# Kernel tuning notes

Hardware: AMD Instinct MI355X
Metric: run time of the kernel (lower is better)

## Reference

```python
import jax, jax.numpy as jnp
import numpy as np

N = 8192
F_IN = 128
F_OUT = 128


def setup_inputs() -> dict:
    key = jax.random.key(0)
    k1, k2, k3, k4, k5 = jax.random.split(key, 5)
    x = jax.random.normal(k1, (N, F_IN), dtype=jnp.float32)
    adj = jax.random.uniform(k2, (N, N), dtype=jnp.float32)
    kernel = jax.random.normal(k3, (F_IN, F_OUT), dtype=jnp.float32) * 0.05
    bias = jax.random.normal(k4, (F_OUT,), dtype=jnp.float32) * 0.05
    beta = jax.random.uniform(k5, (N,), dtype=jnp.float32)
    return {"x": x, "adj": adj, "kernel": kernel, "bias": bias, "beta": beta}


def reference(x, adj, kernel, bias, beta):
    # torch: diag(1/(adj.sum(1)+beta)) @ (adj + diag(beta)) @ x @ kernel + bias
    # (adj + diag(beta)) @ x  ==  adj @ x + beta[:, None] * x  (no NxN temp)
    inv_deg = 1.0 / (jnp.sum(adj, axis=1) + beta)        # [N]
    agg = adj @ x + beta[:, None] * x                     # [N, F_in]
    out = (inv_deg[:, None] * agg) @ kernel + bias        # [N, F_out]
    return out
```

## Files before the change

kernel.cpp:

```cpp
#include <hip/hip_runtime.h>

#define NN 8192
#define FD 128
#define BK 128
#define NRING 4

typedef float f32x4 __attribute__((ext_vector_type(4)));
typedef short short8 __attribute__((ext_vector_type(8)));
typedef unsigned short ushort4v __attribute__((ext_vector_type(4)));
typedef unsigned short ushort8v __attribute__((ext_vector_type(8)));
typedef unsigned int uint4v __attribute__((ext_vector_type(4)));

__device__ __forceinline__ unsigned short f2bf(float f) {
  unsigned int u = __builtin_bit_cast(unsigned int, f);
  u += 0x7fffu + ((u >> 16) & 1u);
  return (unsigned short)(u >> 16);
}
__device__ __forceinline__ float bf2f(unsigned short h) {
  unsigned int u = ((unsigned int)h) << 16;
  return __builtin_bit_cast(float, u);
}

__global__ __launch_bounds__(256) void xk_kernel(
    const float* __restrict__ x, const float* __restrict__ kern,
    unsigned short* __restrict__ bfrag, unsigned short* __restrict__ xk_rm) {
  __shared__ __align__(16) unsigned short kl[FD * FD];
  __shared__ __align__(16) float xl[16 * FD];
  const int t = threadIdx.x;
  const int row0 = blockIdx.x * 16;

  #pragma unroll
  for (int j = 0; j < 16; ++j) {
    int idx = (j * 256 + t) * 4;
    f32x4 kv = *(const f32x4*)&kern[idx];
    ushort4v kw;
    #pragma unroll
    for (int q = 0; q < 4; ++q) kw[q] = f2bf(kv[q]);
    *(ushort4v*)&kl[idx] = kw;
  }
  #pragma unroll
  for (int j = 0; j < 2; ++j) {
    int idx = (j * 256 + t) * 4;
    *(f32x4*)&xl[idx] = *(const f32x4*)&x[(size_t)row0 * FD + idx];
  }
  __syncthreads();

  const int r0 = (t >> 5) * 2;
  const int c0 = (t & 31) * 4;
  float acc[2][4] = {};
  #pragma unroll 4
  for (int k = 0; k < FD; ++k) {
    ushort4v kq = *(const ushort4v*)&kl[k * FD + c0];
    float kv[4];
    #pragma unroll
    for (int q = 0; q < 4; ++q) kv[q] = bf2f(kq[q]);
    float x0 = xl[r0 * FD + k];
    float x1 = xl[(r0 + 1) * FD + k];
    #pragma unroll
    for (int q = 0; q < 4; ++q) {
      acc[0][q] += x0 * kv[q];
      acc[1][q] += x1 * kv[q];
    }
  }
  #pragma unroll
  for (int i = 0; i < 2; ++i) {
    const int r = row0 + r0 + i;
    const int kt = r >> 5;
    const int lhi = ((r >> 3) & 3) * 16;
    const int j = r & 7;
    ushort4v ow;
    #pragma unroll
    for (int q = 0; q < 4; ++q) {
      const int c = c0 + q;
      unsigned short bv = f2bf(acc[i][q]);
      ow[q] = bv;
      bfrag[(((size_t)kt * 8 + (c >> 4)) * 64 + (lhi + (c & 15))) * 8 + j] = bv;
    }
    *(ushort4v*)&xk_rm[(size_t)r * FD + c0] = ow;
  }
}

#define DMA_A(stp, buf)                                                       \
  do {                                                                        \
    _Pragma("unroll") for (int c = 0; c < 4; ++c) {                           \
      const float* g = ag[c] + (size_t)(stp) * BK;                            \
      __builtin_amdgcn_global_load_lds(                                       \
          (const __attribute__((address_space(1))) void*)g,                   \
          (__attribute__((address_space(3))) void*)                           \
              &ring[buf][(w * 4 + c) * 256],                                  \
          16, 0, 0);                                                          \
    }                                                                         \
  } while (0)

#define LOAD_B(stp, Bf)                                                       \
  do {                                                                        \
    const int ktg = kt0 + (stp) * 4;                                          \
    _Pragma("unroll") for (int kk = 0; kk < 4; ++kk)                          \
      _Pragma("unroll") for (int ci = 0; ci < 2; ++ci)                        \
        Bf[kk * 2 + ci] = *(const ushort8v*)(bp +                             \
            (((size_t)(ktg + kk) * 8 + (w * 2 + ci)) << 9));                  \
  } while (0)

#define WAITBAR()                                                             \
  do {                                                                        \
    asm volatile("s_waitcnt vmcnt(12)" ::: "memory");                         \
    __builtin_amdgcn_sched_barrier(0);                                        \
    __builtin_amdgcn_s_barrier();                                             \
    __builtin_amdgcn_sched_barrier(0);                                        \
  } while (0)

#define CONSUME(buf, Bf)                                                      \
  do {                                                                        \
    const float* sb = &ring[buf][0];                                          \
    _Pragma("unroll") for (int kk = 0; kk < 4; ++kk) {                        \
      short8 aF[2];                                                           \
      _Pragma("unroll") for (int mf = 0; mf < 2; ++mf) {                      \
        const int row = (l & 15) + 16 * mf;                                   \
        const int u0 = (l >> 4) * 2 + kk * 8;                                 \
        f32x4 lo = *(const f32x4*)&sb[row * BK + ((u0 ^ (row & 7)) * 4)];     \
        f32x4 hi = *(const f32x4*)&sb[row * BK + (((u0 + 1) ^ (row & 7)) * 4)];\
        unsigned int w0, w1, w2, w3;                                          \
        asm("v_cvt_pk_bf16_f32 %0, %1, %2" : "=v"(w0) : "v"(lo[0]), "v"(lo[1]));\
        asm("v_cvt_pk_bf16_f32 %0, %1, %2" : "=v"(w1) : "v"(lo[2]), "v"(lo[3]));\
        asm("v_cvt_pk_bf16_f32 %0, %1, %2" : "=v"(w2) : "v"(hi[0]), "v"(hi[1]));\
        asm("v_cvt_pk_bf16_f32 %0, %1, %2" : "=v"(w3) : "v"(hi[2]), "v"(hi[3]));\
        uint4v uw = {w0, w1, w2, w3};                                         \
        aF[mf] = __builtin_bit_cast(short8, uw);                              \
        if (kk == w)                                                          \
          rs[mf] += lo[0] + lo[1] + lo[2] + lo[3] +                           \
                    hi[0] + hi[1] + hi[2] + hi[3];                            \
      }                                                                       \
      _Pragma("unroll") for (int mf = 0; mf < 2; ++mf)                        \
        _Pragma("unroll") for (int ci = 0; ci < 2; ++ci)                      \
          acc[mf][ci] = __builtin_amdgcn_mfma_f32_16x16x32_bf16(              \
              aF[mf], Bf[kk * 2 + ci], acc[mf][ci], 0, 0, 0);                 \
    }                                                                         \
  } while (0)

template <int S>
__global__ __launch_bounds__(256, 2) void gcn_mm(
    const float* __restrict__ adj, const unsigned short* __restrict__ bfrag,
    unsigned short* __restrict__ parts, float* __restrict__ rowpart) {
  constexpr int KW = NN / S;
  constexpr int NS = KW / BK;
  static_assert(NS >= 4 && (NS % 2) == 0, "ring needs NS>=4 even");
  __shared__ float ring[NRING][32 * BK];
  __shared__ float rsx[4][2][16];

  const int t = threadIdx.x;
  const int l = t & 63;
  const int w = t >> 6;
  const int b = blockIdx.x;
  const int s = b & (S - 1);
  const int row0 = (b / S) * 32;
  const int kbase = s * KW;
  const int kt0 = s * (KW / 32);

  const float* ag[4];
  #pragma unroll
  for (int c = 0; c < 4; ++c) {
    const int row = 8 * w + 2 * c + (l >> 5);
    const int u = (l & 31) ^ (row & 7);
    ag[c] = adj + (size_t)(row0 + row) * NN + kbase + u * 4;
  }
  const unsigned short* bp = bfrag + (size_t)l * 8;

  ushort8v BfA[8], BfB[8];
  f32x4 acc[2][2] = {};
  float rs[2] = {0.f, 0.f};

  DMA_A(0, 0);
  DMA_A(1, 1);
  DMA_A(2, 2);
  LOAD_B(0, BfA);

  for (int j = 0; j < NS; j += 2) {
    LOAD_B((j + 1 < NS ? j + 1 : NS - 1), BfB);
    WAITBAR();
    if (j + 3 < NS) DMA_A(j + 3, (j + 3) & 3);
    __builtin_amdgcn_sched_barrier(0);
    CONSUME(j & 3, BfA);
    LOAD_B((j + 2 < NS ? j + 2 : NS - 1), BfA);
    WAITBAR();
    if (j + 4 < NS) DMA_A(j + 4, (j + 4) & 3);
    __builtin_amdgcn_sched_barrier(0);
    CONSUME((j + 1) & 3, BfB);
  }

  #pragma unroll
  for (int mf = 0; mf < 2; ++mf) {
    rs[mf] += __shfl_xor(rs[mf], 16);
    rs[mf] += __shfl_xor(rs[mf], 32);
  }
  if (l < 16) {
    rsx[w][0][l] = rs[0];
    rsx[w][1][l] = rs[1];
  }
  __syncthreads();
  if (t < 32) {
    float tot = rsx[0][t >> 4][t & 15] + rsx[1][t >> 4][t & 15] +
                rsx[2][t >> 4][t & 15] + rsx[3][t >> 4][t & 15];
    rowpart[(size_t)s * NN + row0 + t] = tot;
  }

  unsigned short* pp = parts + ((size_t)s * NN + row0) * FD + w * 32;
  #pragma unroll
  for (int mf = 0; mf < 2; ++mf)
    #pragma unroll
    for (int ci = 0; ci < 2; ++ci)
      #pragma unroll
      for (int jj = 0; jj < 4; ++jj) {
        const int r = mf * 16 + ((l >> 4) << 2) + jj;
        pp[(size_t)r * FD + ci * 16 + (l & 15)] = f2bf(acc[mf][ci][jj]);
      }
}

__global__ __launch_bounds__(256) void gcn_fin(
    const unsigned short* __restrict__ parts, const float* __restrict__ rowpart,
    const unsigned short* __restrict__ xk_rm, const float* __restrict__ beta,
    const float* __restrict__ bias, float* __restrict__ out, int S) {
  const int t = threadIdx.x;
  const int r = blockIdx.x * 16 + (t >> 4);
  const int c0 = (t & 15) * 8;

  float rsum = 0.f;
  for (int s = 0; s < S; ++s) rsum += rowpart[(size_t)s * NN + r];
  const float bt = beta[r];
  const float inv = 1.0f / (rsum + bt);

  float a[8] = {0.f, 0.f, 0.f, 0.f, 0.f, 0.f, 0.f, 0.f};
  for (int s = 0; s < S; ++s) {
    ushort8v pv = *(const ushort8v*)&parts[((size_t)s * NN + r) * FD + c0];
    #pragma unroll
    for (int q = 0; q < 8; ++q) a[q] += bf2f(pv[q]);
  }
  ushort8v xv = *(const ushort8v*)&xk_rm[(size_t)r * FD + c0];
  f32x4 o0, o1;
  #pragma unroll
  for (int q = 0; q < 4; ++q) {
    o0[q] = (a[q] + bt * bf2f(xv[q])) * inv + bias[c0 + q];
    o1[q] = (a[4 + q] + bt * bf2f(xv[4 + q])) * inv + bias[c0 + 4 + q];
  }
  *(f32x4*)&out[(size_t)r * FD + c0] = o0;
  *(f32x4*)&out[(size_t)r * FD + c0 + 4] = o1;
}

extern "C" void kernel_launch(void* const* d_in, const int* in_sizes, int n_in,
                              void* d_out, int out_size, void* d_ws, size_t ws_size,
                              hipStream_t stream) {
  const float* x    = (const float*)d_in[0];
  const float* adj  = (const float*)d_in[1];
  const float* kern = (const float*)d_in[2];
  const float* bias = (const float*)d_in[3];
  const float* beta = (const float*)d_in[4];
  float* out = (float*)d_out;

  char* ws = (char*)d_ws;
  unsigned short* bfrag = (unsigned short*)ws;
  unsigned short* xk_rm = (unsigned short*)(ws + (size_t)NN * FD * 2);
  const size_t off_rowpart = (size_t)NN * FD * 4;
  float* rowpart = (float*)(ws + off_rowpart);
  const size_t off_parts = off_rowpart + (size_t)8 * NN * 4;
  unsigned short* parts = (unsigned short*)(ws + off_parts);

  int S = 8;
  while (S > 1 && off_parts + (size_t)S * NN * FD * 2 > ws_size) S >>= 1;

  hipLaunchKernelGGL(xk_kernel, dim3(NN / 16), dim3(256), 0, stream,
                     x, kern, bfrag, xk_rm);

  dim3 blk(256);
  switch (S) {
    case 8: hipLaunchKernelGGL(gcn_mm<8>, dim3(256 * 8), blk, 0, stream, adj, bfrag, parts, rowpart); break;
    case 4: hipLaunchKernelGGL(gcn_mm<4>, dim3(256 * 4), blk, 0, stream, adj, bfrag, parts, rowpart); break;
    case 2: hipLaunchKernelGGL(gcn_mm<2>, dim3(256 * 2), blk, 0, stream, adj, bfrag, parts, rowpart); break;
    default: hipLaunchKernelGGL(gcn_mm<1>, dim3(256), blk, 0, stream, adj, bfrag, parts, rowpart); break;
  }

  hipLaunchKernelGGL(gcn_fin, dim3(NN / 16), dim3(256), 0, stream,
                     parts, rowpart, xk_rm, beta, bias, out, S);
}
```

Measured before the change: 87.44 us.

## Deepen B-fragment prefetch to three stages and raise priority around MFMAs

The main K loop is fully unrolled for the NS==8 case. It now keeps three register sets of B fragments in flight alongside the 4-slot LDS ring for A, so global loads for B are issued three steps ahead. The vmcnt waits are adjusted to match, with the tail steps draining explicitly. s_setprio is raised around the MFMA groups to favour the matrix instructions when waves contend. The cost is more VGPRs from the third B buffer, which may hurt occupancy under launch_bounds(256,2), and a slower fallback path for other split counts.

```diff
diff --git a/kernel.cpp b/kernel.cpp
--- a/kernel.cpp
+++ b/kernel.cpp
@@ -79,6 +79,8 @@
     *(ushort4v*)&xk_rm[(size_t)r * FD + c0] = ow;
   }
 }
+
+#define WAITV(n) asm volatile("s_waitcnt vmcnt(" #n ")" ::: "memory")
 
 #define DMA_A(stp, buf)                                                       \
   do {                                                                        \
@@ -101,17 +103,16 @@
             (((size_t)(ktg + kk) * 8 + (w * 2 + ci)) << 9));                  \
   } while (0)
 
-#define WAITBAR()                                                             \
-  do {                                                                        \
-    asm volatile("s_waitcnt vmcnt(12)" ::: "memory");                         \
+#define BARRIER3()                                                            \
+  do {                                                                        \
     __builtin_amdgcn_sched_barrier(0);                                        \
     __builtin_amdgcn_s_barrier();                                             \
     __builtin_amdgcn_sched_barrier(0);                                        \
   } while (0)
 
-#define CONSUME(buf, Bf)                                                      \
-  do {                                                                        \
-    const float* sb = &ring[buf][0];                                          \
+#define CONSUME(bidx, Bf)                                                     \
+  do {                                                                        \
+    const float* sb = &ring[bidx][0];                                         \
     _Pragma("unroll") for (int kk = 0; kk < 4; ++kk) {                        \
       short8 aF[2];                                                           \
       _Pragma("unroll") for (int mf = 0; mf < 2; ++mf) {                      \
@@ -130,11 +131,30 @@
           rs[mf] += lo[0] + lo[1] + lo[2] + lo[3] +                           \
                     hi[0] + hi[1] + hi[2] + hi[3];                            \
       }                                                                       \
+      __builtin_amdgcn_s_setprio(1);                                          \
       _Pragma("unroll") for (int mf = 0; mf < 2; ++mf)                        \
         _Pragma("unroll") for (int ci = 0; ci < 2; ++ci)                      \
           acc[mf][ci] = __builtin_amdgcn_mfma_f32_16x16x32_bf16(              \
               aF[mf], Bf[kk * 2 + ci], acc[mf][ci], 0, 0, 0);                 \
+      __builtin_amdgcn_s_setprio(0);                                          \
     }                                                                         \
+  } while (0)
+
+#define ITER_FULL(j, Bset)                                                    \
+  do {                                                                        \
+    WAITV(24);                                                                \
+    BARRIER3();                                                               \
+    DMA_A((j) + 3, ((j) + 3) & 3);                                            \
+    __builtin_amdgcn_sched_barrier(0);                                        \
+    CONSUME((j) & 3, Bset);                                                   \
+    LOAD_B((j) + 3, Bset);                                                    \
+  } while (0)
+
+#define ITER_TAIL(j, Bset, WMACRO)                                            \
+  do {                                                                        \
+    WMACRO;                                                                   \
+    BARRIER3();                                                               \
+    CONSUME((j) & 3, Bset);                                                   \
   } while (0)
 
 template <int S>
@@ -143,7 +163,6 @@
     unsigned short* __restrict__ parts, float* __restrict__ rowpart) {
   constexpr int KW = NN / S;
   constexpr int NS = KW / BK;
-  static_assert(NS >= 4 && (NS % 2) == 0, "ring needs NS>=4 even");
   __shared__ float ring[NRING][32 * BK];
   __shared__ float rsx[4][2][16];
 
@@ -165,26 +184,31 @@
   }
   const unsigned short* bp = bfrag + (size_t)l * 8;
 
-  ushort8v BfA[8], BfB[8];
+  ushort8v Bf0[8], Bf1[8], Bf2[8];
   f32x4 acc[2][2] = {};
   float rs[2] = {0.f, 0.f};
 
-  DMA_A(0, 0);
-  DMA_A(1, 1);
-  DMA_A(2, 2);
-  LOAD_B(0, BfA);
-
-  for (int j = 0; j < NS; j += 2) {
-    LOAD_B((j + 1 < NS ? j + 1 : NS - 1), BfB);
-    WAITBAR();
-    if (j + 3 < NS) DMA_A(j + 3, (j + 3) & 3);
-    __builtin_amdgcn_sched_barrier(0);
-    CONSUME(j & 3, BfA);
-    LOAD_B((j + 2 < NS ? j + 2 : NS - 1), BfA);
-    WAITBAR();
-    if (j + 4 < NS) DMA_A(j + 4, (j + 4) & 3);
-    __builtin_amdgcn_sched_barrier(0);
-    CONSUME((j + 1) & 3, BfB);
+  if constexpr (NS == 8) {
+    DMA_A(0, 0); LOAD_B(0, Bf0);
+    DMA_A(1, 1); LOAD_B(1, Bf1);
+    DMA_A(2, 2); LOAD_B(2, Bf2);
+    ITER_FULL(0, Bf0);
+    ITER_FULL(1, Bf1);
+    ITER_FULL(2, Bf2);
+    ITER_FULL(3, Bf0);
+    ITER_FULL(4, Bf1);
+    ITER_TAIL(5, Bf2, WAITV(24));
+    ITER_TAIL(6, Bf0, WAITV(12));
+    ITER_TAIL(7, Bf1, WAITV(0));
+  } else {
+    DMA_A(0, 0);
+    for (int j = 0; j < NS; ++j) {
+      LOAD_B(j, Bf0);
+      WAITV(0);
+      BARRIER3();
+      if (j + 1 < NS) DMA_A(j + 1, (j + 1) & 3);
+      CONSUME(j & 3, Bf0);
+    }
   }
 
   #pragma unroll
```

New measurement: 88.76 us. Within noise of the previous version (+1.5%).
